# Kernel optimization log

Hardware: AMD Instinct MI355X
Metric: run time of the kernel (lower is better)

## Reference

```python
import jax, jax.numpy as jnp
import numpy as np

NUM_VECTORS = 8192
DIM = 64

def setup_inputs() -> dict:
    key = jax.random.key(0)
    kx, kw = jax.random.split(key)
    x = jax.random.normal(kx, (8, 4096, DIM), dtype=jnp.float32)
    W = jax.random.normal(kw, (NUM_VECTORS, DIM), dtype=jnp.float32)
    return {"x": x, "W": W}

def reference(x, W):
    # x: [B, S, C] channels_last (ndim==3 -> channels_first=False)
    shape = x.shape
    flat = x.reshape(-1, shape[-1])  # [N, C]
    # cdist + argmin: argmin of squared euclidean distance is identical to argmin of cdist
    x2 = jnp.sum(flat * flat, axis=1, keepdims=True)          # [N, 1]
    w2 = jnp.sum(W * W, axis=1)                                # [K]
    d2 = x2 - 2.0 * (flat @ W.T) + w2                          # [N, K] dominant intermediate
    indices = jnp.argmin(d2, axis=1)                           # [N]
    z = W[indices]                                             # gather [N, C]
    # losses (use_ema=True -> codebook_loss = 0)
    commitment_loss = jnp.mean((z - jax.lax.stop_gradient(flat)) ** 2)
    codebook_loss = jnp.zeros_like(commitment_loss)
    # straight-through estimator
    z_st = flat + jax.lax.stop_gradient(z - flat)
    # perplexity: scatter one-hot counts -> mean -> entropy
    n = flat.shape[0]
    counts = jnp.zeros((NUM_VECTORS,), dtype=jnp.float32).at[indices].add(1.0)
    avg_probs = counts / n
    perplexity = jnp.exp(-jnp.sum(avg_probs * jnp.log(avg_probs + 1e-10)))
    z_out = z_st.reshape(shape)
    return (z_out, codebook_loss, commitment_loss, perplexity)
```

## Files before the change

kernel.cpp:

```cpp
#include <hip/hip_runtime.h>
#include <math.h>

#define N_ROWS 32768
#define K_CODES 8192
#define DIM 64
#define CHUNKS 4
#define CPC (K_CODES / CHUNKS)
#define TILES (CPC / 32)

using half8  = __attribute__((ext_vector_type(8))) _Float16;
using f32x16 = __attribute__((ext_vector_type(16))) float;

#define WS_W2     0
#define WS_COUNTS 32768
#define WS_CSUM   65536
#define WS_BEST   65552
#define WS_WHL    327936

__device__ __forceinline__ void gload_lds16(const _Float16* g, _Float16* l) {
    __builtin_amdgcn_global_load_lds(
        (const __attribute__((address_space(1))) void*)g,
        (__attribute__((address_space(3))) void*)l, 16, 0, 0);
}

__global__ __launch_bounds__(256) void vq_prep(const float* __restrict__ W,
                                               _Float16* __restrict__ whl,
                                               float* __restrict__ w2g,
                                               unsigned long long* __restrict__ best,
                                               int* __restrict__ counts,
                                               float* __restrict__ csum) {
    int g = blockIdx.x * 256 + threadIdx.x;
    int code = g >> 6, k = g & 63;
    float w = W[g];
    _Float16 h  = (_Float16)w;
    _Float16 lo = (_Float16)(w - (float)h);
    whl[(size_t)code * 128 + k]      = h;
    whl[(size_t)code * 128 + 64 + k] = lo;
    float s = w * w;
    #pragma unroll
    for (int off = 32; off; off >>= 1) s += __shfl_down(s, off);
    if (k == 0) w2g[code] = s;
    if (g < N_ROWS)  best[g] = ~0ULL;
    if (g < K_CODES) counts[g] = 0;
    if (g == 0)      *csum = 0.f;
}

__global__ __launch_bounds__(256, 2) void vq_mfma(const float* __restrict__ x,
                                                  const _Float16* __restrict__ whl,
                                                  const float* __restrict__ w2g,
                                                  unsigned long long* __restrict__ best) {
    __shared__ __align__(16) _Float16 lds[4][4096];
    __shared__ float w2l[CPC];

    const int t     = threadIdx.x;
    const int wv    = t >> 6;
    const int l     = t & 63;
    const int ln31  = l & 31;
    const int lhalf = l >> 5;
    const int chunk = blockIdx.x & (CHUNKS - 1);
    const int rblk  = blockIdx.x / CHUNKS;
    const int rowb  = rblk * 256 + wv * 64;
    const int cbase = chunk * CPC;

    for (int i = t; i < CPC; i += 256) w2l[i] = w2g[cbase + i];

    half8 ahi0[4], alo0[4], ahi1[4], alo1[4];
    {
        const float* xr0 = x + (size_t)(rowb + ln31) * DIM + lhalf * 8;
        const float* xr1 = x + (size_t)(rowb + 32 + ln31) * DIM + lhalf * 8;
        #pragma unroll
        for (int kt = 0; kt < 4; ++kt) {
            float4 a0 = *(const float4*)(xr0 + kt * 16);
            float4 a1 = *(const float4*)(xr0 + kt * 16 + 4);
            float4 b0 = *(const float4*)(xr1 + kt * 16);
            float4 b1 = *(const float4*)(xr1 + kt * 16 + 4);
            float fa[8] = {a0.x, a0.y, a0.z, a0.w, a1.x, a1.y, a1.z, a1.w};
            float fb[8] = {b0.x, b0.y, b0.z, b0.w, b1.x, b1.y, b1.z, b1.w};
            #pragma unroll
            for (int j = 0; j < 8; ++j) {
                _Float16 h0 = (_Float16)fa[j];
                _Float16 h1 = (_Float16)fb[j];
                ahi0[kt][j] = h0; alo0[kt][j] = (_Float16)(fa[j] - (float)h0);
                ahi1[kt][j] = h1; alo1[kt][j] = (_Float16)(fb[j] - (float)h1);
            }
        }
    }

    const _Float16* srcp[2];
    int ldsG[2];
    #pragma unroll
    for (int p = 0; p < 2; ++p) {
        int q = p * 4 + wv;
        srcp[p] = whl + (size_t)(cbase + ln31) * 128 + ((q & 1) * 8 + lhalf + 2 * (q >> 1)) * 8;
        ldsG[p] = (p * 256 + wv * 64) * 8;
    }

    float bv0[16], bv1[16];
    int   bi0[16], bi1[16];
    #pragma unroll
    for (int s2 = 0; s2 < 16; ++s2) { bv0[s2] = 3.4e38f; bv1[s2] = 3.4e38f; bi0[s2] = 0; bi1[s2] = 0; }

    __syncthreads();

    #pragma unroll
    for (int pre = 0; pre < 3; ++pre)
        #pragma unroll
        for (int p = 0; p < 2; ++p)
            gload_lds16(srcp[p] + pre * 4096, &lds[0][0] + pre * 4096 + ldsG[p]);

#define TILE_BODY(WAITN, DO_PF, tt)                                              \
  {                                                                              \
    asm volatile("s_waitcnt vmcnt(" #WAITN ")" ::: "memory");                    \
    __builtin_amdgcn_s_barrier();                                                \
    if (DO_PF) {                                                                 \
      _Pragma("unroll")                                                          \
      for (int p = 0; p < 2; ++p)                                                \
        gload_lds16(srcp[p] + ((tt) + 3) * 4096,                                 \
                    &lds[0][0] + (((tt) + 3) & 3) * 4096 + ldsG[p]);             \
    }                                                                            \
    const _Float16* lb = &lds[0][0] + ((tt) & 3) * 4096;                         \
    float w2v = w2l[(tt) * 32 + ln31];                                           \
    f32x16 acc0 = {}, acc1 = {};                                                 \
    __builtin_amdgcn_s_setprio(1);                                               \
    _Pragma("unroll")                                                            \
    for (int kt = 0; kt < 4; ++kt) {                                             \
      half8 bh = *(const half8*)(lb + ((kt * 2 + 0) * 64 + l) * 8);              \
      half8 bl = *(const half8*)(lb + ((kt * 2 + 1) * 64 + l) * 8);              \
      acc0 = __builtin_amdgcn_mfma_f32_32x32x16_f16(ahi0[kt], bh, acc0, 0, 0, 0);\
      acc1 = __builtin_amdgcn_mfma_f32_32x32x16_f16(ahi1[kt], bh, acc1, 0, 0, 0);\
      acc0 = __builtin_amdgcn_mfma_f32_32x32x16_f16(alo0[kt], bh, acc0, 0, 0, 0);\
      acc1 = __builtin_amdgcn_mfma_f32_32x32x16_f16(alo1[kt], bh, acc1, 0, 0, 0);\
      acc0 = __builtin_amdgcn_mfma_f32_32x32x16_f16(ahi0[kt], bl, acc0, 0, 0, 0);\
      acc1 = __builtin_amdgcn_mfma_f32_32x32x16_f16(ahi1[kt], bl, acc1, 0, 0, 0);\
    }                                                                            \
    __builtin_amdgcn_s_setprio(0);                                               \
    const int cc = cbase + (tt) * 32 + ln31;                                     \
    _Pragma("unroll")                                                            \
    for (int s2 = 0; s2 < 16; ++s2) {                                            \
      float sA = fmaf(-2.f, acc0[s2], w2v);                                      \
      float sB = fmaf(-2.f, acc1[s2], w2v);                                      \
      if (sA < bv0[s2]) { bv0[s2] = sA; bi0[s2] = cc; }                          \
      if (sB < bv1[s2]) { bv1[s2] = sB; bi1[s2] = cc; }                          \
    }                                                                            \
  }

    for (int tile = 0; tile < TILES - 3; ++tile)
        TILE_BODY(4, true, tile);
    TILE_BODY(4, false, TILES - 3);
    TILE_BODY(2, false, TILES - 2);
    TILE_BODY(0, false, TILES - 1);
#undef TILE_BODY

    #pragma unroll
    for (int rg = 0; rg < 2; ++rg) {
        #pragma unroll
        for (int s2 = 0; s2 < 16; ++s2) {
            float fv = rg ? bv1[s2] : bv0[s2];
            int   iv = rg ? bi1[s2] : bi0[s2];
            unsigned uk = __float_as_uint(fv);
            uk = (uk >> 31) ? ~uk : (uk | 0x80000000u);
            unsigned long long key = ((unsigned long long)uk << 32) | (unsigned)iv;
            #pragma unroll
            for (int off = 16; off; off >>= 1) {
                unsigned long long o = __shfl_xor(key, off);
                key = (o < key) ? o : key;
            }
            if (ln31 == 0) {
                int rl = (s2 & 3) + 8 * (s2 >> 2) + 4 * lhalf;
                atomicMin(&best[rowb + rg * 32 + rl], key);
            }
        }
    }
}

__global__ __launch_bounds__(256) void vq_gather(const float* __restrict__ x,
                                                 const float* __restrict__ W,
                                                 const unsigned long long* __restrict__ best,
                                                 float* __restrict__ zout,
                                                 int* __restrict__ counts,
                                                 float* __restrict__ csum) {
    int t   = threadIdx.x;
    int row = blockIdx.x * 64 + (t >> 2);
    int seg = t & 3;
    int idx = (int)(best[row] & 0xFFFFFFFFULL);
    if (seg == 0) atomicAdd(&counts[idx], 1);
    const float* wrow = W    + (size_t)idx * DIM + seg * 16;
    const float* xrow = x    + (size_t)row * DIM + seg * 16;
    float*       zrow = zout + (size_t)row * DIM + seg * 16;
    float local = 0.f;
    #pragma unroll
    for (int j = 0; j < 16; j += 4) {
        float4 wv = *(const float4*)(wrow + j);
        float4 xv = *(const float4*)(xrow + j);
        *(float4*)(zrow + j) = wv;
        float dx = wv.x - xv.x, dy = wv.y - xv.y, dz = wv.z - xv.z, dw = wv.w - xv.w;
        local += dx * dx + dy * dy + dz * dz + dw * dw;
    }
    #pragma unroll
    for (int off = 32; off; off >>= 1) local += __shfl_down(local, off);
    if ((t & 63) == 0) atomicAdd(csum, local);
}

__global__ __launch_bounds__(256) void vq_final(const int* __restrict__ counts,
                                                const float* __restrict__ csum,
                                                float* __restrict__ out3) {
    __shared__ float sh[4];
    float e = 0.f;
    for (int i = threadIdx.x; i < K_CODES; i += 256) {
        float p = (float)counts[i] * (1.0f / N_ROWS);
        e += p * logf(p + 1e-10f);
    }
    #pragma unroll
    for (int off = 32; off; off >>= 1) e += __shfl_down(e, off);
    if ((threadIdx.x & 63) == 0) sh[threadIdx.x >> 6] = e;
    __syncthreads();
    if (threadIdx.x == 0) {
        float tot = sh[0] + sh[1] + sh[2] + sh[3];
        out3[0] = 0.f;
        out3[1] = csum[0] * (1.0f / ((float)N_ROWS * DIM));
        out3[2] = expf(-tot);
    }
}

extern "C" void kernel_launch(void* const* d_in, const int* in_sizes, int n_in,
                              void* d_out, int out_size, void* d_ws, size_t ws_size,
                              hipStream_t stream) {
    (void)in_sizes; (void)n_in; (void)out_size; (void)ws_size;
    const float* x = (const float*)d_in[0];
    const float* W = (const float*)d_in[1];
    float* zout = (float*)d_out;
    float* out3 = (float*)d_out + (size_t)N_ROWS * DIM;

    float*              w2g    = (float*)((char*)d_ws + WS_W2);
    int*                counts = (int*)((char*)d_ws + WS_COUNTS);
    float*              csum   = (float*)((char*)d_ws + WS_CSUM);
    unsigned long long* best   = (unsigned long long*)((char*)d_ws + WS_BEST);
    _Float16*           whl    = (_Float16*)((char*)d_ws + WS_WHL);

    vq_prep  <<<K_CODES * DIM / 256,   256, 0, stream>>>(W, whl, w2g, best, counts, csum);
    vq_mfma  <<<(N_ROWS / 256) * CHUNKS, 256, 0, stream>>>(x, whl, w2g, best);
    vq_gather<<<N_ROWS / 64,           256, 0, stream>>>(x, W, best, zout, counts, csum);
    vq_final <<<1,                     256, 0, stream>>>(counts, csum, out3);
}
```

Before: 159.7 us.

## Double the codebook chunks, raise occupancy, and switch to a two-buffer LDS pipeline

Splits the codebook into 8 chunks instead of 4, which doubles the grid. The launch bound rises to 4 blocks per CU to increase occupancy. The 4-stage LDS prefetch ring, with its manual vmcnt waits and barriers, becomes a simple double buffer synchronised with __syncthreads once per tile. The per-block LDS copy of the squared codebook norms is dropped, and norms are read directly from global memory. Together these cut LDS use per block. The risks are register spills from the tighter launch bound (the kernel keeps a large set of A fragments and best-value registers live), less load-latency hiding, and twice as many atomicMin merges.

Result: slower. 356.2 us (+123.0%).

```diff
diff --git a/kernel.cpp b/kernel.cpp
--- a/kernel.cpp
+++ b/kernel.cpp
@@ -4,7 +4,7 @@
 #define N_ROWS 32768
 #define K_CODES 8192
 #define DIM 64
-#define CHUNKS 4
+#define CHUNKS 8
 #define CPC (K_CODES / CHUNKS)
 #define TILES (CPC / 32)
 
@@ -45,12 +45,11 @@
     if (g == 0)      *csum = 0.f;
 }
 
-__global__ __launch_bounds__(256, 2) void vq_mfma(const float* __restrict__ x,
+__global__ __launch_bounds__(256, 4) void vq_mfma(const float* __restrict__ x,
                                                   const _Float16* __restrict__ whl,
                                                   const float* __restrict__ w2g,
                                                   unsigned long long* __restrict__ best) {
-    __shared__ __align__(16) _Float16 lds[4][4096];
-    __shared__ float w2l[CPC];
+    __shared__ __align__(16) _Float16 lds[2][4096];
 
     const int t     = threadIdx.x;
     const int wv    = t >> 6;
@@ -61,8 +60,6 @@
     const int rblk  = blockIdx.x / CHUNKS;
     const int rowb  = rblk * 256 + wv * 64;
     const int cbase = chunk * CPC;
-
-    for (int i = t; i < CPC; i += 256) w2l[i] = w2g[cbase + i];
 
     half8 ahi0[4], alo0[4], ahi1[4], alo1[4];
     {
@@ -100,56 +97,48 @@
     #pragma unroll
     for (int s2 = 0; s2 < 16; ++s2) { bv0[s2] = 3.4e38f; bv1[s2] = 3.4e38f; bi0[s2] = 0; bi1[s2] = 0; }
 
+    #pragma unroll
+    for (int p = 0; p < 2; ++p) gload_lds16(srcp[p], &lds[0][0] + ldsG[p]);
     __syncthreads();
 
-    #pragma unroll
-    for (int pre = 0; pre < 3; ++pre)
-        #pragma unroll
-        for (int p = 0; p < 2; ++p)
-            gload_lds16(srcp[p] + pre * 4096, &lds[0][0] + pre * 4096 + ldsG[p]);
-
-#define TILE_BODY(WAITN, DO_PF, tt)                                              \
-  {                                                                              \
-    asm volatile("s_waitcnt vmcnt(" #WAITN ")" ::: "memory");                    \
-    __builtin_amdgcn_s_barrier();                                                \
-    if (DO_PF) {                                                                 \
-      _Pragma("unroll")                                                          \
-      for (int p = 0; p < 2; ++p)                                                \
-        gload_lds16(srcp[p] + ((tt) + 3) * 4096,                                 \
-                    &lds[0][0] + (((tt) + 3) & 3) * 4096 + ldsG[p]);             \
-    }                                                                            \
-    const _Float16* lb = &lds[0][0] + ((tt) & 3) * 4096;                         \
-    float w2v = w2l[(tt) * 32 + ln31];                                           \
-    f32x16 acc0 = {}, acc1 = {};                                                 \
-    __builtin_amdgcn_s_setprio(1);                                               \
-    _Pragma("unroll")                                                            \
-    for (int kt = 0; kt < 4; ++kt) {                                             \
-      half8 bh = *(const half8*)(lb + ((kt * 2 + 0) * 64 + l) * 8);              \
-      half8 bl = *(const half8*)(lb + ((kt * 2 + 1) * 64 + l) * 8);              \
-      acc0 = __builtin_amdgcn_mfma_f32_32x32x16_f16(ahi0[kt], bh, acc0, 0, 0, 0);\
-      acc1 = __builtin_amdgcn_mfma_f32_32x32x16_f16(ahi1[kt], bh, acc1, 0, 0, 0);\
-      acc0 = __builtin_amdgcn_mfma_f32_32x32x16_f16(alo0[kt], bh, acc0, 0, 0, 0);\
-      acc1 = __builtin_amdgcn_mfma_f32_32x32x16_f16(alo1[kt], bh, acc1, 0, 0, 0);\
-      acc0 = __builtin_amdgcn_mfma_f32_32x32x16_f16(ahi0[kt], bl, acc0, 0, 0, 0);\
-      acc1 = __builtin_amdgcn_mfma_f32_32x32x16_f16(ahi1[kt], bl, acc1, 0, 0, 0);\
-    }                                                                            \
-    __builtin_amdgcn_s_setprio(0);                                               \
-    const int cc = cbase + (tt) * 32 + ln31;                                     \
-    _Pragma("unroll")                                                            \
-    for (int s2 = 0; s2 < 16; ++s2) {                                            \
-      float sA = fmaf(-2.f, acc0[s2], w2v);                                      \
-      float sB = fmaf(-2.f, acc1[s2], w2v);                                      \
-      if (sA < bv0[s2]) { bv0[s2] = sA; bi0[s2] = cc; }                          \
-      if (sB < bv1[s2]) { bv1[s2] = sB; bi1[s2] = cc; }                          \
-    }                                                                            \
-  }
-
-    for (int tile = 0; tile < TILES - 3; ++tile)
-        TILE_BODY(4, true, tile);
-    TILE_BODY(4, false, TILES - 3);
-    TILE_BODY(2, false, TILES - 2);
-    TILE_BODY(0, false, TILES - 1);
-#undef TILE_BODY
+    const float* w2p = w2g + cbase + ln31;
+    int cur = 0;
+
+    for (int tile = 0; tile < TILES; ++tile) {
+        if (tile < TILES - 1) {
+            #pragma unroll
+            for (int p = 0; p < 2; ++p)
+                gload_lds16(srcp[p] + (tile + 1) * 4096, &lds[0][0] + (cur ^ 1) * 4096 + ldsG[p]);
+        }
+        const float w2v = w2p[tile * 32];
+        const _Float16* lb = &lds[0][0] + cur * 4096;
+
+        f32x16 acc0 = {}, acc1 = {};
+        __builtin_amdgcn_s_setprio(1);
+        #pragma unroll
+        for (int kt = 0; kt < 4; ++kt) {
+            half8 bh = *(const half8*)(lb + ((kt * 2 + 0) * 64 + l) * 8);
+            half8 bl = *(const half8*)(lb + ((kt * 2 + 1) * 64 + l) * 8);
+            acc0 = __builtin_amdgcn_mfma_f32_32x32x16_f16(ahi0[kt], bh, acc0, 0, 0, 0);
+            acc1 = __builtin_amdgcn_mfma_f32_32x32x16_f16(ahi1[kt], bh, acc1, 0, 0, 0);
+            acc0 = __builtin_amdgcn_mfma_f32_32x32x16_f16(alo0[kt], bh, acc0, 0, 0, 0);
+            acc1 = __builtin_amdgcn_mfma_f32_32x32x16_f16(alo1[kt], bh, acc1, 0, 0, 0);
+            acc0 = __builtin_amdgcn_mfma_f32_32x32x16_f16(ahi0[kt], bl, acc0, 0, 0, 0);
+            acc1 = __builtin_amdgcn_mfma_f32_32x32x16_f16(ahi1[kt], bl, acc1, 0, 0, 0);
+        }
+        __builtin_amdgcn_s_setprio(0);
+
+        const int cc = cbase + tile * 32 + ln31;
+        #pragma unroll
+        for (int s2 = 0; s2 < 16; ++s2) {
+            float sA = fmaf(-2.f, acc0[s2], w2v);
+            float sB = fmaf(-2.f, acc1[s2], w2v);
+            if (sA < bv0[s2]) { bv0[s2] = sA; bi0[s2] = cc; }
+            if (sB < bv1[s2]) { bv1[s2] = sB; bi1[s2] = cc; }
+        }
+        __syncthreads();
+        cur ^= 1;
+    }
 
     #pragma unroll
     for (int rg = 0; rg < 2; ++rg) {
@@ -237,8 +226,8 @@
     unsigned long long* best   = (unsigned long long*)((char*)d_ws + WS_BEST);
     _Float16*           whl    = (_Float16*)((char*)d_ws + WS_WHL);
 
-    vq_prep  <<<K_CODES * DIM / 256,   256, 0, stream>>>(W, whl, w2g, best, counts, csum);
+    vq_prep  <<<K_CODES * DIM / 256,     256, 0, stream>>>(W, whl, w2g, best, counts, csum);
     vq_mfma  <<<(N_ROWS / 256) * CHUNKS, 256, 0, stream>>>(x, whl, w2g, best);
-    vq_gather<<<N_ROWS / 64,           256, 0, stream>>>(x, W, best, zout, counts, csum);
-    vq_final <<<1,                     256, 0, stream>>>(counts, csum, out3);
-}
+    vq_gather<<<N_ROWS / 64,             256, 0, stream>>>(x, W, best, zout, counts, csum);
+    vq_final <<<1,                       256, 0, stream>>>(counts, csum, out3);
+}
```

## Fold -2 scaling and w2 bias into MFMA, per-wave LDS staging, cheaper loss

Applied to the files above, without the earlier changes.

Prescales the codebook by -2 and adds ||w||^2 (split into hi/lo fp16) through an extra MFMA with a ones vector, so the epilogue no longer needs fmaf. The shared 4-slot LDS pipeline with block-wide barriers becomes a per-wave double buffer with no barriers, and the next tile is staged after the MFMAs. Adds the lo*lo MFMA terms, which costs extra MFMA work per tile. The commitment loss is computed from precomputed ||x||^2 plus the decoded best score, so the gather kernel no longer reads x.

Result: slower. 187.9 us (+17.6%).

```diff
diff --git a/kernel.cpp b/kernel.cpp
--- a/kernel.cpp
+++ b/kernel.cpp
@@ -11,11 +11,12 @@
 using half8  = __attribute__((ext_vector_type(8))) _Float16;
 using f32x16 = __attribute__((ext_vector_type(16))) float;
 
-#define WS_W2     0
+#define WS_W2HL   0
 #define WS_COUNTS 32768
 #define WS_CSUM   65536
 #define WS_BEST   65552
-#define WS_WHL    327936
+#define WS_X2     327696
+#define WS_WM2    458768
 
 __device__ __forceinline__ void gload_lds16(const _Float16* g, _Float16* l) {
     __builtin_amdgcn_global_load_lds(
@@ -24,33 +25,47 @@
 }
 
 __global__ __launch_bounds__(256) void vq_prep(const float* __restrict__ W,
-                                               _Float16* __restrict__ whl,
-                                               float* __restrict__ w2g,
+                                               const float* __restrict__ x,
+                                               _Float16* __restrict__ wm2hl,
+                                               unsigned* __restrict__ w2hl,
+                                               float* __restrict__ x2g,
                                                unsigned long long* __restrict__ best,
                                                int* __restrict__ counts,
                                                float* __restrict__ csum) {
     int g = blockIdx.x * 256 + threadIdx.x;
     int code = g >> 6, k = g & 63;
     float w = W[g];
-    _Float16 h  = (_Float16)w;
-    _Float16 lo = (_Float16)(w - (float)h);
-    whl[(size_t)code * 128 + k]      = h;
-    whl[(size_t)code * 128 + 64 + k] = lo;
+    float wm2 = -2.0f * w;
+    _Float16 h  = (_Float16)wm2;
+    _Float16 lo = (_Float16)(wm2 - (float)h);
+    wm2hl[(size_t)code * 128 + k]      = h;
+    wm2hl[(size_t)code * 128 + 64 + k] = lo;
     float s = w * w;
     #pragma unroll
     for (int off = 32; off; off >>= 1) s += __shfl_down(s, off);
-    if (k == 0) w2g[code] = s;
+    if (k == 0) {
+        _Float16 wh = (_Float16)s;
+        _Float16 wl = (_Float16)(s - (float)wh);
+        unsigned pk = (unsigned)(unsigned short)__builtin_bit_cast(unsigned short, wh)
+                    | ((unsigned)(unsigned short)__builtin_bit_cast(unsigned short, wl) << 16);
+        w2hl[code] = pk;
+    }
+    float4 xv = *(const float4*)(x + (size_t)g * 4);
+    float ss = xv.x * xv.x + xv.y * xv.y + xv.z * xv.z + xv.w * xv.w;
+    #pragma unroll
+    for (int off = 8; off; off >>= 1) ss += __shfl_down(ss, off);
+    if ((g & 15) == 0) x2g[g >> 4] = ss;
     if (g < N_ROWS)  best[g] = ~0ULL;
     if (g < K_CODES) counts[g] = 0;
     if (g == 0)      *csum = 0.f;
 }
 
 __global__ __launch_bounds__(256, 2) void vq_mfma(const float* __restrict__ x,
-                                                  const _Float16* __restrict__ whl,
-                                                  const float* __restrict__ w2g,
+                                                  const _Float16* __restrict__ wm2hl,
+                                                  const unsigned* __restrict__ w2g,
                                                   unsigned long long* __restrict__ best) {
-    __shared__ __align__(16) _Float16 lds[4][4096];
-    __shared__ float w2l[CPC];
+    __shared__ __align__(16) _Float16 lds[4][2][4096];
+    __shared__ unsigned w2lds[CPC];
 
     const int t     = threadIdx.x;
     const int wv    = t >> 6;
@@ -62,7 +77,7 @@
     const int rowb  = rblk * 256 + wv * 64;
     const int cbase = chunk * CPC;
 
-    for (int i = t; i < CPC; i += 256) w2l[i] = w2g[cbase + i];
+    for (int i = t; i < CPC; i += 256) w2lds[i] = w2g[cbase + i];
 
     half8 ahi0[4], alo0[4], ahi1[4], alo1[4];
     {
@@ -86,14 +101,13 @@
         }
     }
 
-    const _Float16* srcp[2];
-    int ldsG[2];
-    #pragma unroll
-    for (int p = 0; p < 2; ++p) {
-        int q = p * 4 + wv;
-        srcp[p] = whl + (size_t)(cbase + ln31) * 128 + ((q & 1) * 8 + lhalf + 2 * (q >> 1)) * 8;
-        ldsG[p] = (p * 256 + wv * 64) * 8;
-    }
+    half8 aw2;
+    #pragma unroll
+    for (int j = 0; j < 8; ++j) aw2[j] = (lhalf == 0 && j < 2) ? (_Float16)1.0f : (_Float16)0.0f;
+
+    const _Float16* srcb = wm2hl + (size_t)(cbase + ln31) * 128 + lhalf * 8;
+    _Float16* slot0 = &lds[wv][0][0];
+    _Float16* slot1 = &lds[wv][1][0];
 
     float bv0[16], bv1[16];
     int   bi0[16], bi1[16];
@@ -102,26 +116,28 @@
 
     __syncthreads();
 
-    #pragma unroll
-    for (int pre = 0; pre < 3; ++pre)
-        #pragma unroll
-        for (int p = 0; p < 2; ++p)
-            gload_lds16(srcp[p] + pre * 4096, &lds[0][0] + pre * 4096 + ldsG[p]);
-
-#define TILE_BODY(WAITN, DO_PF, tt)                                              \
+#define STAGE(tt, sl)                                                            \
+    { _Pragma("unroll")                                                          \
+      for (int p = 0; p < 8; ++p)                                                \
+          gload_lds16(srcb + (size_t)(tt) * 4096 + (p & 1) * 64 + (p >> 1) * 16, \
+                      (sl) + p * 512); }
+
+    STAGE(0, slot0)
+    STAGE(1, slot1)
+
+#define TILE_BODY(VM, DO_STAGE, tt)                                              \
   {                                                                              \
-    asm volatile("s_waitcnt vmcnt(" #WAITN ")" ::: "memory");                    \
-    __builtin_amdgcn_s_barrier();                                                \
-    if (DO_PF) {                                                                 \
-      _Pragma("unroll")                                                          \
-      for (int p = 0; p < 2; ++p)                                                \
-        gload_lds16(srcp[p] + ((tt) + 3) * 4096,                                 \
-                    &lds[0][0] + (((tt) + 3) & 3) * 4096 + ldsG[p]);             \
-    }                                                                            \
-    const _Float16* lb = &lds[0][0] + ((tt) & 3) * 4096;                         \
-    float w2v = w2l[(tt) * 32 + ln31];                                           \
+    asm volatile("s_waitcnt vmcnt(" #VM ")" ::: "memory");                       \
+    _Float16* sb = ((tt) & 1) ? slot1 : slot0;                                   \
+    const _Float16* lb = sb;                                                     \
+    unsigned pk = w2lds[(tt) * 32 + ln31];                                       \
+    unsigned v0 = (lhalf == 0) ? pk : 0u;                                        \
+    union { half8 h8; unsigned u[4]; } bw2u;                                     \
+    bw2u.u[0] = v0; bw2u.u[1] = 0; bw2u.u[2] = 0; bw2u.u[3] = 0;                 \
     f32x16 acc0 = {}, acc1 = {};                                                 \
     __builtin_amdgcn_s_setprio(1);                                               \
+    acc0 = __builtin_amdgcn_mfma_f32_32x32x16_f16(aw2, bw2u.h8, acc0, 0, 0, 0);  \
+    acc1 = __builtin_amdgcn_mfma_f32_32x32x16_f16(aw2, bw2u.h8, acc1, 0, 0, 0);  \
     _Pragma("unroll")                                                            \
     for (int kt = 0; kt < 4; ++kt) {                                             \
       half8 bh = *(const half8*)(lb + ((kt * 2 + 0) * 64 + l) * 8);              \
@@ -131,25 +147,28 @@
       acc0 = __builtin_amdgcn_mfma_f32_32x32x16_f16(alo0[kt], bh, acc0, 0, 0, 0);\
       acc1 = __builtin_amdgcn_mfma_f32_32x32x16_f16(alo1[kt], bh, acc1, 0, 0, 0);\
       acc0 = __builtin_amdgcn_mfma_f32_32x32x16_f16(ahi0[kt], bl, acc0, 0, 0, 0);\
+      acc1 = __builtin_amdgcn_mfma_f32_32x32x16_f16(alo1[kt], bl, acc1, 0, 0, 0);\
       acc1 = __builtin_amdgcn_mfma_f32_32x32x16_f16(ahi1[kt], bl, acc1, 0, 0, 0);\
+      acc0 = __builtin_amdgcn_mfma_f32_32x32x16_f16(alo0[kt], bl, acc0, 0, 0, 0);\
     }                                                                            \
     __builtin_amdgcn_s_setprio(0);                                               \
+    __builtin_amdgcn_sched_barrier(0);                                           \
+    if (DO_STAGE) { STAGE((tt) + 2, sb) }                                        \
     const int cc = cbase + (tt) * 32 + ln31;                                     \
     _Pragma("unroll")                                                            \
     for (int s2 = 0; s2 < 16; ++s2) {                                            \
-      float sA = fmaf(-2.f, acc0[s2], w2v);                                      \
-      float sB = fmaf(-2.f, acc1[s2], w2v);                                      \
+      float sA = acc0[s2];                                                       \
+      float sB = acc1[s2];                                                       \
       if (sA < bv0[s2]) { bv0[s2] = sA; bi0[s2] = cc; }                          \
       if (sB < bv1[s2]) { bv1[s2] = sB; bi1[s2] = cc; }                          \
     }                                                                            \
   }
 
-    for (int tile = 0; tile < TILES - 3; ++tile)
-        TILE_BODY(4, true, tile);
-    TILE_BODY(4, false, TILES - 3);
-    TILE_BODY(2, false, TILES - 2);
+    for (int tile = 0; tile < TILES - 1; ++tile)
+        TILE_BODY(8, (tile + 2 < TILES), tile);
     TILE_BODY(0, false, TILES - 1);
 #undef TILE_BODY
+#undef STAGE
 
     #pragma unroll
     for (int rg = 0; rg < 2; ++rg) {
@@ -173,28 +192,29 @@
     }
 }
 
-__global__ __launch_bounds__(256) void vq_gather(const float* __restrict__ x,
-                                                 const float* __restrict__ W,
+__global__ __launch_bounds__(256) void vq_gather(const float* __restrict__ W,
                                                  const unsigned long long* __restrict__ best,
+                                                 const float* __restrict__ x2g,
                                                  float* __restrict__ zout,
                                                  int* __restrict__ counts,
                                                  float* __restrict__ csum) {
     int t   = threadIdx.x;
     int row = blockIdx.x * 64 + (t >> 2);
     int seg = t & 3;
-    int idx = (int)(best[row] & 0xFFFFFFFFULL);
-    if (seg == 0) atomicAdd(&counts[idx], 1);
+    unsigned long long key = best[row];
+    int idx = (int)(key & 0xFFFFFFFFULL);
+
     const float* wrow = W    + (size_t)idx * DIM + seg * 16;
-    const float* xrow = x    + (size_t)row * DIM + seg * 16;
     float*       zrow = zout + (size_t)row * DIM + seg * 16;
+    #pragma unroll
+    for (int j = 0; j < 16; j += 4) *(float4*)(zrow + j) = *(const float4*)(wrow + j);
+
     float local = 0.f;
-    #pragma unroll
-    for (int j = 0; j < 16; j += 4) {
-        float4 wv = *(const float4*)(wrow + j);
-        float4 xv = *(const float4*)(xrow + j);
-        *(float4*)(zrow + j) = wv;
-        float dx = wv.x - xv.x, dy = wv.y - xv.y, dz = wv.z - xv.z, dw = wv.w - xv.w;
-        local += dx * dx + dy * dy + dz * dz + dw * dw;
+    if (seg == 0) {
+        atomicAdd(&counts[idx], 1);
+        unsigned uk = (unsigned)(key >> 32);
+        unsigned ob = (uk & 0x80000000u) ? (uk & 0x7FFFFFFFu) : ~uk;
+        local = x2g[row] + __uint_as_float(ob);
     }
     #pragma unroll
     for (int off = 32; off; off >>= 1) local += __shfl_down(local, off);
@@ -231,14 +251,15 @@
     float* zout = (float*)d_out;
     float* out3 = (float*)d_out + (size_t)N_ROWS * DIM;
 
-    float*              w2g    = (float*)((char*)d_ws + WS_W2);
+    unsigned*           w2hl   = (unsigned*)((char*)d_ws + WS_W2HL);
     int*                counts = (int*)((char*)d_ws + WS_COUNTS);
     float*              csum   = (float*)((char*)d_ws + WS_CSUM);
     unsigned long long* best   = (unsigned long long*)((char*)d_ws + WS_BEST);
-    _Float16*           whl    = (_Float16*)((char*)d_ws + WS_WHL);
-
-    vq_prep  <<<K_CODES * DIM / 256,   256, 0, stream>>>(W, whl, w2g, best, counts, csum);
-    vq_mfma  <<<(N_ROWS / 256) * CHUNKS, 256, 0, stream>>>(x, whl, w2g, best);
-    vq_gather<<<N_ROWS / 64,           256, 0, stream>>>(x, W, best, zout, counts, csum);
-    vq_final <<<1,                     256, 0, stream>>>(counts, csum, out3);
-}
+    float*              x2g    = (float*)((char*)d_ws + WS_X2);
+    _Float16*           wm2hl  = (_Float16*)((char*)d_ws + WS_WM2);
+
+    vq_prep  <<<K_CODES * DIM / 256,     256, 0, stream>>>(W, x, wm2hl, w2hl, x2g, best, counts, csum);
+    vq_mfma  <<<(N_ROWS / 256) * CHUNKS, 256, 0, stream>>>(x, wm2hl, w2hl, best);
+    vq_gather<<<N_ROWS / 64,             256, 0, stream>>>(W, best, x2g, zout, counts, csum);
+    vq_final <<<1,                       256, 0, stream>>>(counts, csum, out3);
+}
```
